# Kernel optimization log

Hardware: AMD Instinct MI355X
Metric: run time of the kernel (lower is better)

Reference implementation:

```python
import jax, jax.numpy as jnp
import numpy as np

N = 100000      # nodes
E = 640000      # directed edges (before self-loops)
F_IN = 128      # num_features
C1 = 64         # latent_size (conv1 out, heads=1)
C2 = 16         # num_classes (conv2 out, heads=1)
NEG_SLOPE = 0.2


def setup_inputs() -> dict:
    key = jax.random.key(0)
    ks = jax.random.split(key, 10)
    s = 0.1
    return {
        "x": jax.random.normal(ks[0], (N, F_IN), jnp.float32),
        "edge_index": jax.random.randint(ks[1], (2, E), 0, N, dtype=jnp.int32),
        "W1": jax.random.normal(ks[2], (F_IN, C1), jnp.float32) * s,
        "att_src1": jax.random.normal(ks[3], (C1,), jnp.float32) * s,
        "att_dst1": jax.random.normal(ks[4], (C1,), jnp.float32) * s,
        "b1": jax.random.normal(ks[5], (C1,), jnp.float32) * s,
        "W2": jax.random.normal(ks[6], (C1, C2), jnp.float32) * s,
        "att_src2": jax.random.normal(ks[7], (C2,), jnp.float32) * s,
        "att_dst2": jax.random.normal(ks[8], (C2,), jnp.float32) * s,
        "b2": jax.random.normal(ks[9], (C2,), jnp.float32) * s,
    }


def gat_layer(x, src, dst, W, a_src, a_dst, b, n_nodes):
    # x: [N, F] -> h: [N, C] (heads=1)
    h = x @ W
    # per-edge attention logits: alpha_j + alpha_i, then leaky_relu
    alpha = jax.nn.leaky_relu((h @ a_src)[src] + (h @ a_dst)[dst], NEG_SLOPE)
    # scatter-softmax over destination-node groups (numerically stable)
    amax = jax.ops.segment_max(alpha, dst, num_segments=n_nodes)
    e = jnp.exp(alpha - amax[dst])
    denom = jax.ops.segment_sum(e, dst, num_segments=n_nodes)
    w = e / (denom[dst] + 1e-16)
    # gather src features, weight, scatter-add to dst
    out = jax.ops.segment_sum(h[src] * w[:, None], dst, num_segments=n_nodes)
    return out + b


def kl_to_std_normal(out):
    # GIB reparameterize: mean = out[:, :ceil(C/2)], std = softplus(out[:, -ceil(C/2):])
    size = (out.shape[-1] + 1) // 2
    mean = out[:, :size]
    std = jax.nn.softplus(out[:, -size:]) + 1e-10
    kl = -jnp.log(std) + 0.5 * (std * std + mean * mean - 1.0)
    return kl.reshape(out.shape[0], -1, 1)  # [N, size, heads=1]


def reference(x, edge_index, W1, att_src1, att_dst1, b1, W2, att_src2, att_dst2, b2):
    n = x.shape[0]
    loop = jnp.arange(n, dtype=edge_index.dtype)  # PyG GATConv add_self_loops=True
    src = jnp.concatenate([edge_index[0], loop])
    dst = jnp.concatenate([edge_index[1], loop])

    out1 = gat_layer(x, src, dst, W1, att_src1, att_dst1, b1, n)
    ixz1 = kl_to_std_normal(out1)

    h = jax.nn.elu(out1)  # dropout is a no-op in eval mode
    out2 = gat_layer(h, src, dst, W2, att_src2, att_dst2, b2, n)
    ixz2 = kl_to_std_normal(out2)

    return (out2, ixz1, ixz2)
```

## Files before the change

kernel.cpp:

```cpp
#include <hip/hip_runtime.h>
#include <math.h>

#define NN 100000
#define NE 640000
#define FIN 128
#define C1 64
#define C2 16
#define NEG_SLOPE 0.2f
#define SLOTS 32
#define G1_BLOCKS ((NN + 127) / 128)
#define SORT_EPB 2048
#define SORT_NBLK ((NE + SORT_EPB - 1) / SORT_EPB)
#define NBUCK 512
#define NBUCK_USED ((NN + 255) / 256)

typedef unsigned int uint32;
typedef __attribute__((ext_vector_type(8))) short bf16x8;
typedef __attribute__((ext_vector_type(4))) float f32x4;

static __device__ __forceinline__ float lrelu(float x) { return x > 0.f ? x : NEG_SLOPE * x; }
static __device__ __forceinline__ float softplusn(float x) {
    return fmaxf(x, 0.f) + __logf(1.f + __expf(-fabsf(x)));
}
static __device__ __forceinline__ unsigned short f2bf(float f) {
    uint32 u = __float_as_uint(f);
    u += 0x7fffu + ((u >> 16) & 1u);
    return (unsigned short)(u >> 16);
}
static __device__ __forceinline__ float bf2f_lo(uint32 p) { return __uint_as_float(p << 16); }
static __device__ __forceinline__ float bf2f_hi(uint32 p) { return __uint_as_float(p & 0xffff0000u); }

#define G1T 2
__global__ __launch_bounds__(256, 3) void k_gemm1(
        const float* __restrict__ x, const float* __restrict__ W1,
        const float* __restrict__ attS, const float* __restrict__ attD,
        unsigned short* __restrict__ h1b, float* __restrict__ as1, float* __restrict__ ad1) {
    __shared__ uint32 ts[4][16][36];
    int lane = threadIdx.x & 63;
    int wv = threadIdx.x >> 6;
    int col = lane & 15;
    int g = lane >> 4;
    int wbase = (blockIdx.x * 4 + wv) * (G1T * 16);
    if (wbase >= NN) return;

    bf16x8 bfr[4][4];
#pragma unroll
    for (int t = 0; t < 4; t++)
#pragma unroll
        for (int j = 0; j < 4; j++) {
            int c = col + j * 16;
#pragma unroll
            for (int i = 0; i < 8; i++)
                bfr[t][j][i] = (short)f2bf(W1[(t * 32 + g * 8 + i) * C1 + c]);
        }
    float ats[4], atd[4];
#pragma unroll
    for (int j = 0; j < 4; j++) { ats[j] = attS[col + j * 16]; atd[j] = attD[col + j * 16]; }

    for (int tl = 0; tl < G1T; tl++) {
        int tbase = wbase + tl * 16;
        int arow = tbase + col; if (arow > NN - 1) arow = NN - 1;
        const float* xr = &x[(size_t)arow * FIN];
        float4 f0[4], f1[4];
#pragma unroll
        for (int t = 0; t < 4; t++) {
            f0[t] = *reinterpret_cast<const float4*>(&xr[t * 32 + g * 8]);
            f1[t] = *reinterpret_cast<const float4*>(&xr[t * 32 + g * 8 + 4]);
        }
        bf16x8 a[4];
#pragma unroll
        for (int t = 0; t < 4; t++) {
            a[t][0] = (short)f2bf(f0[t].x); a[t][1] = (short)f2bf(f0[t].y);
            a[t][2] = (short)f2bf(f0[t].z); a[t][3] = (short)f2bf(f0[t].w);
            a[t][4] = (short)f2bf(f1[t].x); a[t][5] = (short)f2bf(f1[t].y);
            a[t][6] = (short)f2bf(f1[t].z); a[t][7] = (short)f2bf(f1[t].w);
        }
        f32x4 acc[4];
#pragma unroll
        for (int j = 0; j < 4; j++) acc[j] = (f32x4){0.f, 0.f, 0.f, 0.f};
#pragma unroll
        for (int t = 0; t < 4; t++)
#pragma unroll
            for (int j = 0; j < 4; j++)
                acc[j] = __builtin_amdgcn_mfma_f32_16x16x32_bf16(a[t], bfr[t][j], acc[j], 0, 0, 0);

        float sA[4] = {0.f, 0.f, 0.f, 0.f}, sD[4] = {0.f, 0.f, 0.f, 0.f};
        unsigned short* tsw = (unsigned short*)&ts[wv][0][0];
#pragma unroll
        for (int reg = 0; reg < 4; reg++) {
            int trow = g * 4 + reg;
#pragma unroll
            for (int j = 0; j < 4; j++) {
                float v = acc[j][reg];
                tsw[trow * 72 + col + j * 16] = f2bf(v);
                sA[reg] = fmaf(v, ats[j], sA[reg]);
                sD[reg] = fmaf(v, atd[j], sD[reg]);
            }
        }
        __builtin_amdgcn_wave_barrier();
        {
            int rrow = lane >> 2, rq = lane & 3;
            uint4 w0 = *reinterpret_cast<const uint4*>(&ts[wv][rrow][rq * 8]);
            uint4 w1 = *reinterpret_cast<const uint4*>(&ts[wv][rrow][rq * 8 + 4]);
            int orow = tbase + rrow;
            if (orow < NN) {
                unsigned short* op = &h1b[(size_t)orow * C1 + rq * 16];
                *reinterpret_cast<uint4*>(op) = w0;
                *reinterpret_cast<uint4*>(op + 8) = w1;
            }
        }
        __builtin_amdgcn_wave_barrier();
#pragma unroll
        for (int off = 8; off; off >>= 1)
#pragma unroll
            for (int reg = 0; reg < 4; reg++) {
                sA[reg] += __shfl_xor(sA[reg], off);
                sD[reg] += __shfl_xor(sD[reg], off);
            }
        if (col == 0) {
#pragma unroll
            for (int reg = 0; reg < 4; reg++) {
                int row = tbase + g * 4 + reg;
                if (row < NN) { as1[row] = sA[reg]; ad1[row] = sD[reg]; }
            }
        }
    }
}

__global__ __launch_bounds__(256) void k_hist(const int* __restrict__ ei, int* __restrict__ blockHist) {
    __shared__ int lh[NBUCK];
    int t = threadIdx.x;
    for (int i = t; i < NBUCK; i += 256) lh[i] = 0;
    __syncthreads();
    int base = blockIdx.x * SORT_EPB;
#pragma unroll
    for (int k = 0; k < 8; k++) {
        int e = base + k * 256 + t;
        if (e < NE) atomicAdd(&lh[ei[NE + e] >> 8], 1);
    }
    __syncthreads();
    for (int i = t; i < NBUCK; i += 256) blockHist[i * SORT_NBLK + blockIdx.x] = lh[i];
}

__global__ __launch_bounds__(256) void k_scan(int* __restrict__ blockHist, int* __restrict__ bucketCnt) {
    __shared__ int s[SORT_NBLK];
    int b = blockIdx.x, t = threadIdx.x;
    for (int i = t; i < SORT_NBLK; i += 256) s[i] = blockHist[b * SORT_NBLK + i];
    __syncthreads();
    for (int d = 1; d < SORT_NBLK; d <<= 1) {
        int i0 = t, i1 = t + 256;
        int v0 = 0, v1 = 0;
        if (i0 >= d && i0 < SORT_NBLK) v0 = s[i0 - d];
        if (i1 >= d && i1 < SORT_NBLK) v1 = s[i1 - d];
        __syncthreads();
        if (i0 >= d && i0 < SORT_NBLK) s[i0] += v0;
        if (i1 >= d && i1 < SORT_NBLK) s[i1] += v1;
        __syncthreads();
    }
    for (int i = t; i < SORT_NBLK; i += 256)
        blockHist[b * SORT_NBLK + i] = (i == 0) ? 0 : s[i - 1];
    if (t == 0) bucketCnt[b] = s[SORT_NBLK - 1];
}

__global__ __launch_bounds__(256) void k_scat1(const int* __restrict__ ei,
        const int* __restrict__ blockHist, uint2* __restrict__ ebuf) {
    __shared__ int lh[NBUCK];
    int t = threadIdx.x;
    for (int i = t; i < NBUCK; i += 256) lh[i] = 0;
    __syncthreads();
    int base = blockIdx.x * SORT_EPB;
#pragma unroll
    for (int k = 0; k < 8; k++) {
        int e = base + k * 256 + t;
        if (e < NE) {
            int src = ei[e], dst = ei[NE + e];
            int bin = dst >> 8;
            int rank = atomicAdd(&lh[bin], 1);
            int pos = bin * SORT_EPB + blockHist[bin * SORT_NBLK + blockIdx.x] + rank;
            ebuf[pos] = make_uint2((uint32)src, (uint32)dst);
        }
    }
}

__global__ __launch_bounds__(256) void k_csr(const uint2* __restrict__ ebuf,
        const int* __restrict__ bucketCnt, int* __restrict__ cnt, int* __restrict__ csr32) {
    __shared__ int lcnt[256];
    __shared__ int lcsr[256 * SLOTS];
    int t = threadIdx.x, b = blockIdx.x;
    if (t < 256) lcnt[t] = 0;
    for (int i = t; i < 256 * SLOTS; i += 256) lcsr[i] = 0;
    __syncthreads();
    int n = bucketCnt[b];
    if (n > SORT_EPB) n = SORT_EPB;
    for (int i = t; i < n; i += 256) {
        uint2 e = ebuf[b * SORT_EPB + i];
        int ln = (int)(e.y & 255u);
        int pos = atomicAdd(&lcnt[ln], 1);
        if (pos < SLOTS) lcsr[ln * SLOTS + pos] = (int)e.x;
    }
    __syncthreads();
    int node0 = b * 256;
    for (int i = t; i < 256 * SLOTS; i += 256) {
        int node = node0 + (i >> 5);
        if (node < NN) csr32[(size_t)node0 * SLOTS + i] = lcsr[i];
    }
    if (node0 + t < NN) cnt[node0 + t] = lcnt[t];
}

__global__ __launch_bounds__(256, 4) void k_agg1(
        const int* __restrict__ cnt, const int* __restrict__ csr32,
        const float* __restrict__ as1, const float* __restrict__ ad1,
        const unsigned short* __restrict__ h1b, const float* __restrict__ b1,
        unsigned short* __restrict__ heb, float* __restrict__ ixz1) {
    int lane = threadIdx.x & 63;
    int wid = (blockIdx.x * blockDim.x + threadIdx.x) >> 6;
    int grp = lane >> 4, gl = lane & 15;
    int gbase = grp << 4;
    int node = wid * 4 + grp;
    if (node >= NN) return;
    int base = node * SLOTS;
    int dcnt = cnt[node];
    int s_l = csr32[base + gl];
    int4 S0 = *reinterpret_cast<const int4*>(&csr32[base]);
    int4 S1 = *reinterpret_cast<const int4*>(&csr32[base + 4]);
    int4 S2 = *reinterpret_cast<const int4*>(&csr32[base + 8]);
    int4 S3 = *reinterpret_cast<const int4*>(&csr32[base + 12]);
    float adn = ad1[node];
    float asn = as1[node];
    float asv = as1[s_l];
    float4 o;

    if (dcnt <= 16) {
        float al = (gl < dcnt) ? lrelu(asv + adn) : -1e30f;
        float wl = __expf(al);
        float den = wl;
#pragma unroll
        for (int off = 8; off; off >>= 1) den += __shfl_xor(den, off);
        float wself = __expf(lrelu(asn + adn));
        den += wself;
        float inv = __builtin_amdgcn_rcpf(den + 1e-16f);
        wl *= inv; wself *= inv;
        const unsigned short* hb = h1b + gl * 4;
        uint2 PS  = *reinterpret_cast<const uint2*>(&hb[(size_t)node * C1]);
        uint2 P0  = *reinterpret_cast<const uint2*>(&hb[(size_t)S0.x * C1]);
        uint2 P1  = *reinterpret_cast<const uint2*>(&hb[(size_t)S0.y * C1]);
        uint2 P2  = *reinterpret_cast<const uint2*>(&hb[(size_t)S0.z * C1]);
        uint2 P3  = *reinterpret_cast<const uint2*>(&hb[(size_t)S0.w * C1]);
        uint2 P4  = *reinterpret_cast<const uint2*>(&hb[(size_t)S1.x * C1]);
        uint2 P5  = *reinterpret_cast<const uint2*>(&hb[(size_t)S1.y * C1]);
        uint2 P6  = *reinterpret_cast<const uint2*>(&hb[(size_t)S1.z * C1]);
        uint2 P7  = *reinterpret_cast<const uint2*>(&hb[(size_t)S1.w * C1]);
        uint2 P8  = *reinterpret_cast<const uint2*>(&hb[(size_t)S2.x * C1]);
        uint2 P9  = *reinterpret_cast<const uint2*>(&hb[(size_t)S2.y * C1]);
        uint2 P10 = *reinterpret_cast<const uint2*>(&hb[(size_t)S2.z * C1]);
        uint2 P11 = *reinterpret_cast<const uint2*>(&hb[(size_t)S2.w * C1]);
        uint2 P12 = *reinterpret_cast<const uint2*>(&hb[(size_t)S3.x * C1]);
        uint2 P13 = *reinterpret_cast<const uint2*>(&hb[(size_t)S3.y * C1]);
        uint2 P14 = *reinterpret_cast<const uint2*>(&hb[(size_t)S3.z * C1]);
        uint2 P15 = *reinterpret_cast<const uint2*>(&hb[(size_t)S3.w * C1]);
        float4 acc;
        acc.x = wself * bf2f_lo(PS.x);
        acc.y = wself * bf2f_hi(PS.x);
        acc.z = wself * bf2f_lo(PS.y);
        acc.w = wself * bf2f_hi(PS.y);
#define ACC1(k, Pk) { float w = __shfl(wl, gbase | k); \
        acc.x = fmaf(w, bf2f_lo(Pk.x), acc.x); acc.y = fmaf(w, bf2f_hi(Pk.x), acc.y); \
        acc.z = fmaf(w, bf2f_lo(Pk.y), acc.z); acc.w = fmaf(w, bf2f_hi(Pk.y), acc.w); }
        ACC1(0, P0)  ACC1(1, P1)  ACC1(2, P2)  ACC1(3, P3)
        ACC1(4, P4)  ACC1(5, P5)  ACC1(6, P6)  ACC1(7, P7)
        ACC1(8, P8)  ACC1(9, P9)  ACC1(10, P10) ACC1(11, P11)
        ACC1(12, P12) ACC1(13, P13) ACC1(14, P14) ACC1(15, P15)
#undef ACC1
        o = acc;
    } else {
        int dcl = dcnt < SLOTS ? dcnt : SLOTS;
        float aself = lrelu(asn + adn);
        float m = aself;
        for (int e = gl; e < dcl; e += 16) m = fmaxf(m, lrelu(as1[csr32[base + e]] + adn));
#pragma unroll
        for (int off = 8; off; off >>= 1) m = fmaxf(m, __shfl_xor(m, off));
        float den = 0.f;
        for (int e = gl; e < dcl; e += 16) den += __expf(lrelu(as1[csr32[base + e]] + adn) - m);
#pragma unroll
        for (int off = 8; off; off >>= 1) den += __shfl_xor(den, off);
        den += __expf(aself - m);
        float inv = __builtin_amdgcn_rcpf(den + 1e-16f);
        float wsf = __expf(aself - m) * inv;
        uint2 ps = *reinterpret_cast<const uint2*>(&h1b[(size_t)node * C1 + gl * 4]);
        float4 acc;
        acc.x = wsf * bf2f_lo(ps.x);
        acc.y = wsf * bf2f_hi(ps.x);
        acc.z = wsf * bf2f_lo(ps.y);
        acc.w = wsf * bf2f_hi(ps.y);
        for (int e = 0; e < dcl; e++) {
            int s = csr32[base + e];
            float wgt = __expf(lrelu(as1[s] + adn) - m) * inv;
            uint2 p = *reinterpret_cast<const uint2*>(&h1b[(size_t)s * C1 + gl * 4]);
            acc.x = fmaf(wgt, bf2f_lo(p.x), acc.x);
            acc.y = fmaf(wgt, bf2f_hi(p.x), acc.y);
            acc.z = fmaf(wgt, bf2f_lo(p.y), acc.z);
            acc.w = fmaf(wgt, bf2f_hi(p.y), acc.w);
        }
        o = acc;
    }
    float4 bv = *reinterpret_cast<const float4*>(&b1[gl * 4]);
    o.x += bv.x; o.y += bv.y; o.z += bv.z; o.w += bv.w;
    float4 he;
    he.x = o.x > 0.f ? o.x : __expf(o.x) - 1.f;
    he.y = o.y > 0.f ? o.y : __expf(o.y) - 1.f;
    he.z = o.z > 0.f ? o.z : __expf(o.z) - 1.f;
    he.w = o.w > 0.f ? o.w : __expf(o.w) - 1.f;
    uint2 hw;
    hw.x = (uint32)f2bf(he.x) | ((uint32)f2bf(he.y) << 16);
    hw.y = (uint32)f2bf(he.z) | ((uint32)f2bf(he.w) << 16);
    *reinterpret_cast<uint2*>(&heb[(size_t)node * C1 + gl * 4]) = hw;
    float4 oth;
    oth.x = __shfl_down(o.x, 8);
    oth.y = __shfl_down(o.y, 8);
    oth.z = __shfl_down(o.z, 8);
    oth.w = __shfl_down(o.w, 8);
    if (gl < 8) {
        float4 kl; float sd;
        sd = softplusn(oth.x) + 1e-10f; kl.x = -__logf(sd) + 0.5f * (sd * sd + o.x * o.x - 1.f);
        sd = softplusn(oth.y) + 1e-10f; kl.y = -__logf(sd) + 0.5f * (sd * sd + o.y * o.y - 1.f);
        sd = softplusn(oth.z) + 1e-10f; kl.z = -__logf(sd) + 0.5f * (sd * sd + o.z * o.z - 1.f);
        sd = softplusn(oth.w) + 1e-10f; kl.w = -__logf(sd) + 0.5f * (sd * sd + o.w * o.w - 1.f);
        *reinterpret_cast<float4*>(&ixz1[(size_t)node * 32 + gl * 4]) = kl;
    }
}

#define G2T 4
__global__ __launch_bounds__(256, 4) void k_gemm2(
        const unsigned short* __restrict__ heb, const float* __restrict__ W2,
        const float* __restrict__ attS, const float* __restrict__ attD,
        unsigned short* __restrict__ h2b, float* __restrict__ as2, float* __restrict__ ad2) {
    int lane = threadIdx.x & 63;
    int wv = threadIdx.x >> 6;
    int col = lane & 15, g = lane >> 4;
    int wbase = (blockIdx.x * 4 + wv) * (G2T * 16);
    if (wbase >= NN) return;
    bf16x8 bfr[2];
#pragma unroll
    for (int t = 0; t < 2; t++)
#pragma unroll
        for (int i = 0; i < 8; i++)
            bfr[t][i] = (short)f2bf(W2[(t * 32 + g * 8 + i) * C2 + col]);
    float ats = attS[col], atd = attD[col];
#pragma unroll
    for (int tl = 0; tl < G2T; tl++) {
        int tbase = wbase + tl * 16;
        if (tbase >= NN) break;
        int arow = tbase + col; if (arow > NN - 1) arow = NN - 1;
        bf16x8 a0 = *reinterpret_cast<const bf16x8*>(&heb[(size_t)arow * C1 + g * 8]);
        bf16x8 a1 = *reinterpret_cast<const bf16x8*>(&heb[(size_t)arow * C1 + 32 + g * 8]);
        f32x4 acc = (f32x4){0.f, 0.f, 0.f, 0.f};
        acc = __builtin_amdgcn_mfma_f32_16x16x32_bf16(a0, bfr[0], acc, 0, 0, 0);
        acc = __builtin_amdgcn_mfma_f32_16x16x32_bf16(a1, bfr[1], acc, 0, 0, 0);
        float sA[4], sD[4];
#pragma unroll
        for (int reg = 0; reg < 4; reg++) {
            int row = tbase + g * 4 + reg;
            if (row < NN) h2b[(size_t)row * C2 + col] = f2bf(acc[reg]);
            sA[reg] = acc[reg] * ats;
            sD[reg] = acc[reg] * atd;
        }
#pragma unroll
        for (int off = 8; off; off >>= 1)
#pragma unroll
            for (int reg = 0; reg < 4; reg++) {
                sA[reg] += __shfl_xor(sA[reg], off);
                sD[reg] += __shfl_xor(sD[reg], off);
            }
        if (col == 0) {
#pragma unroll
            for (int reg = 0; reg < 4; reg++) {
                int row = tbase + g * 4 + reg;
                if (row < NN) { as2[row] = sA[reg]; ad2[row] = sD[reg]; }
            }
        }
    }
}

__global__ __launch_bounds__(256, 8) void k_agg2(
        const int* __restrict__ cnt, const int* __restrict__ csr32,
        const float* __restrict__ as2, const float* __restrict__ ad2,
        const unsigned short* __restrict__ h2b, const float* __restrict__ b2,
        float* __restrict__ out2, float* __restrict__ ixz2) {
    int lane = threadIdx.x & 63;
    int wid = (blockIdx.x * blockDim.x + threadIdx.x) >> 6;
    int grp = lane >> 4, gl = lane & 15;
    int gbase = grp << 4;
    int node = wid * 4 + grp;
    if (node >= NN) return;
    int base = node * SLOTS;
    int f4 = gl & 3, eg = gl >> 2;
    int dcnt = cnt[node];
    int s_l = csr32[base + gl];
    int sk0 = csr32[base + eg];
    int sk1 = csr32[base + 4 + eg];
    int sk2 = csr32[base + 8 + eg];
    int sk3 = csr32[base + 12 + eg];
    float adn = ad2[node];
    float asn = as2[node];
    float asv = as2[s_l];
    float out;

    if (dcnt <= 16) {
        float al = (gl < dcnt) ? lrelu(asv + adn) : -1e30f;
        float wl = __expf(al);
        float den = wl;
#pragma unroll
        for (int off = 8; off; off >>= 1) den += __shfl_xor(den, off);
        float wself = __expf(lrelu(asn + adn));
        den += wself;
        float inv = __builtin_amdgcn_rcpf(den + 1e-16f);
        wl *= inv; wself *= inv;
        uint2 PS = *reinterpret_cast<const uint2*>(&h2b[(size_t)node * C2 + f4 * 4]);
        uint2 P0 = *reinterpret_cast<const uint2*>(&h2b[(size_t)sk0 * C2 + f4 * 4]);
        uint2 P1 = *reinterpret_cast<const uint2*>(&h2b[(size_t)sk1 * C2 + f4 * 4]);
        uint2 P2 = *reinterpret_cast<const uint2*>(&h2b[(size_t)sk2 * C2 + f4 * 4]);
        uint2 P3 = *reinterpret_cast<const uint2*>(&h2b[(size_t)sk3 * C2 + f4 * 4]);
        float ws = (eg == 0) ? wself : 0.f;
        float4 acc;
        acc.x = ws * bf2f_lo(PS.x);
        acc.y = ws * bf2f_hi(PS.x);
        acc.z = ws * bf2f_lo(PS.y);
        acc.w = ws * bf2f_hi(PS.y);
        float w0 = __shfl(wl, gbase | eg);
        float w1 = __shfl(wl, gbase | (4 + eg));
        float w2 = __shfl(wl, gbase | (8 + eg));
        float w3 = __shfl(wl, gbase | (12 + eg));
        acc.x = fmaf(w0, bf2f_lo(P0.x), acc.x);
        acc.y = fmaf(w0, bf2f_hi(P0.x), acc.y);
        acc.z = fmaf(w0, bf2f_lo(P0.y), acc.z);
        acc.w = fmaf(w0, bf2f_hi(P0.y), acc.w);
        acc.x = fmaf(w1, bf2f_lo(P1.x), acc.x);
        acc.y = fmaf(w1, bf2f_hi(P1.x), acc.y);
        acc.z = fmaf(w1, bf2f_lo(P1.y), acc.z);
        acc.w = fmaf(w1, bf2f_hi(P1.y), acc.w);
        acc.x = fmaf(w2, bf2f_lo(P2.x), acc.x);
        acc.y = fmaf(w2, bf2f_hi(P2.x), acc.y);
        acc.z = fmaf(w2, bf2f_lo(P2.y), acc.z);
        acc.w = fmaf(w2, bf2f_hi(P2.y), acc.w);
        acc.x = fmaf(w3, bf2f_lo(P3.x), acc.x);
        acc.y = fmaf(w3, bf2f_hi(P3.x), acc.y);
        acc.z = fmaf(w3, bf2f_lo(P3.y), acc.z);
        acc.w = fmaf(w3, bf2f_hi(P3.y), acc.w);
#pragma unroll
        for (int off = 4; off <= 8; off <<= 1) {
            acc.x += __shfl_xor(acc.x, off);
            acc.y += __shfl_xor(acc.y, off);
            acc.z += __shfl_xor(acc.z, off);
            acc.w += __shfl_xor(acc.w, off);
        }
        int srcl = gbase | (gl >> 2);
        float t0 = __shfl(acc.x, srcl);
        float t1 = __shfl(acc.y, srcl);
        float t2 = __shfl(acc.z, srcl);
        float t3 = __shfl(acc.w, srcl);
        float t01 = (gl & 1) ? t1 : t0;
        float t23 = (gl & 1) ? t3 : t2;
        out = (gl & 2) ? t23 : t01;
    } else {
        int dcl = dcnt < SLOTS ? dcnt : SLOTS;
        float aself = lrelu(asn + adn);
        float m = aself;
        for (int e = gl; e < dcl; e += 16) m = fmaxf(m, lrelu(as2[csr32[base + e]] + adn));
#pragma unroll
        for (int off = 8; off; off >>= 1) m = fmaxf(m, __shfl_xor(m, off));
        float den = 0.f;
        for (int e = gl; e < dcl; e += 16) den += __expf(lrelu(as2[csr32[base + e]] + adn) - m);
#pragma unroll
        for (int off = 8; off; off >>= 1) den += __shfl_xor(den, off);
        den += __expf(aself - m);
        float inv = __builtin_amdgcn_rcpf(den + 1e-16f);
        float wsf = __expf(aself - m) * inv;
        float acc = wsf * __uint_as_float(((uint32)h2b[(size_t)node * C2 + gl]) << 16);
        for (int e = 0; e < dcl; e++) {
            int s = csr32[base + e];
            float wgt = __expf(lrelu(as2[s] + adn) - m) * inv;
            acc = fmaf(wgt, __uint_as_float(((uint32)h2b[(size_t)s * C2 + gl]) << 16), acc);
        }
        out = acc;
    }
    out += b2[gl];
    out2[(size_t)node * C2 + gl] = out;
    float other = __shfl_down(out, 8);
    if (gl < 8) {
        float sd = softplusn(other) + 1e-10f;
        float kl = -__logf(sd) + 0.5f * (sd * sd + out * out - 1.f);
        ixz2[(size_t)node * 8 + gl] = kl;
    }
}

extern "C" void kernel_launch(void* const* d_in, const int* in_sizes, int n_in,
                              void* d_out, int out_size, void* d_ws, size_t ws_size,
                              hipStream_t stream) {
    const float* x     = (const float*)d_in[0];
    const int*   ei    = (const int*)d_in[1];
    const float* W1    = (const float*)d_in[2];
    const float* aS1   = (const float*)d_in[3];
    const float* aD1   = (const float*)d_in[4];
    const float* b1    = (const float*)d_in[5];
    const float* W2    = (const float*)d_in[6];
    const float* aS2   = (const float*)d_in[7];
    const float* aD2   = (const float*)d_in[8];
    const float* b2    = (const float*)d_in[9];

    float* out = (float*)d_out;
    float* out2 = out;
    float* ixz1 = out + (size_t)NN * C2;
    float* ixz2 = ixz1 + (size_t)NN * 32;

    char* p = (char*)d_ws;
    auto alloc = [&](size_t bytes) -> void* {
        void* r = (void*)p;
        p += (bytes + 255) & ~(size_t)255;
        return r;
    };
    int* cnt        = (int*)alloc((size_t)NN * 4);
    int* csr32      = (int*)alloc((size_t)NN * SLOTS * 4);
    int* blockHist  = (int*)alloc((size_t)NBUCK * SORT_NBLK * 4);
    int* bucketCnt  = (int*)alloc((size_t)NBUCK * 4);
    uint2* ebuf     = (uint2*)alloc((size_t)NBUCK * SORT_EPB * 8);
    unsigned short* h1b = (unsigned short*)alloc((size_t)NN * C1 * 2);
    float* as1   = (float*)alloc((size_t)NN * 4);
    float* ad1   = (float*)alloc((size_t)NN * 4);
    unsigned short* heb = (unsigned short*)alloc((size_t)NN * C1 * 2);
    unsigned short* h2b = (unsigned short*)alloc((size_t)NN * C2 * 2);
    float* as2   = (float*)alloc((size_t)NN * 4);
    float* ad2   = (float*)alloc((size_t)NN * 4);
    (void)ws_size; (void)in_sizes; (void)n_in; (void)out_size;

    k_gemm1<<<G1_BLOCKS, 256, 0, stream>>>(x, W1, aS1, aD1, h1b, as1, ad1);

    k_hist <<<SORT_NBLK, 256, 0, stream>>>(ei, blockHist);
    k_scan <<<NBUCK, 256, 0, stream>>>(blockHist, bucketCnt);
    k_scat1<<<SORT_NBLK, 256, 0, stream>>>(ei, blockHist, ebuf);
    k_csr  <<<NBUCK_USED, 256, 0, stream>>>(ebuf, bucketCnt, cnt, csr32);

    k_agg1<<<(NN + 15) / 16, 256, 0, stream>>>(cnt, csr32, as1, ad1, h1b, b1, heb, ixz1);

    k_gemm2<<<(NN + 4 * G2T * 16 - 1) / (4 * G2T * 16), 256, 0, stream>>>(heb, W2, aS2, aD2, h2b, as2, ad2);
    k_agg2<<<(NN + 15) / 16, 256, 0, stream>>>(cnt, csr32, as2, ad2, h2b, b2, out2, ixz2);
}
```

Measured before the change: 106.2 us.

## Fuse edge histogram into GEMM1 launch and pack edge buffer entries to 32 bits

The histogram kernel now runs as extra blocks appended to the first GEMM launch, which removes one kernel launch and lets the two independent workloads overlap. The scatter kernel seeds its shared-memory counters with the per-block offsets, so it no longer re-reads the global offset table for every edge. Each edge is packed into one 32-bit word (source shifted left by 8, low 8 bits of the destination), which halves the intermediate buffer's traffic. The shared-memory histogram array raises the GEMM blocks' LDS footprint, which could lower their occupancy, and the packing relies on source ids fitting in 24 bits.

```diff
diff --git a/kernel.cpp b/kernel.cpp
--- a/kernel.cpp
+++ b/kernel.cpp
@@ -31,11 +31,28 @@
 static __device__ __forceinline__ float bf2f_hi(uint32 p) { return __uint_as_float(p & 0xffff0000u); }
 
 #define G1T 2
-__global__ __launch_bounds__(256, 3) void k_gemm1(
+__global__ __launch_bounds__(256, 3) void k_g1hist(
         const float* __restrict__ x, const float* __restrict__ W1,
         const float* __restrict__ attS, const float* __restrict__ attD,
-        unsigned short* __restrict__ h1b, float* __restrict__ as1, float* __restrict__ ad1) {
+        unsigned short* __restrict__ h1b, float* __restrict__ as1, float* __restrict__ ad1,
+        const int* __restrict__ ei, int* __restrict__ blockHist) {
     __shared__ uint32 ts[4][16][36];
+    __shared__ int lh[NBUCK];
+    if (blockIdx.x >= G1_BLOCKS) {
+        int blk = (int)blockIdx.x - G1_BLOCKS;
+        int t = threadIdx.x;
+        for (int i = t; i < NBUCK; i += 256) lh[i] = 0;
+        __syncthreads();
+        int base = blk * SORT_EPB;
+#pragma unroll
+        for (int k = 0; k < 8; k++) {
+            int e = base + k * 256 + t;
+            if (e < NE) atomicAdd(&lh[ei[NE + e] >> 8], 1);
+        }
+        __syncthreads();
+        for (int i = t; i < NBUCK; i += 256) blockHist[i * SORT_NBLK + blk] = lh[i];
+        return;
+    }
     int lane = threadIdx.x & 63;
     int wv = threadIdx.x >> 6;
     int col = lane & 15;
@@ -125,21 +142,6 @@
             }
         }
     }
-}
-
-__global__ __launch_bounds__(256) void k_hist(const int* __restrict__ ei, int* __restrict__ blockHist) {
-    __shared__ int lh[NBUCK];
-    int t = threadIdx.x;
-    for (int i = t; i < NBUCK; i += 256) lh[i] = 0;
-    __syncthreads();
-    int base = blockIdx.x * SORT_EPB;
-#pragma unroll
-    for (int k = 0; k < 8; k++) {
-        int e = base + k * 256 + t;
-        if (e < NE) atomicAdd(&lh[ei[NE + e] >> 8], 1);
-    }
-    __syncthreads();
-    for (int i = t; i < NBUCK; i += 256) blockHist[i * SORT_NBLK + blockIdx.x] = lh[i];
 }
 
 __global__ __launch_bounds__(256) void k_scan(int* __restrict__ blockHist, int* __restrict__ bucketCnt) {
@@ -163,10 +165,10 @@
 }
 
 __global__ __launch_bounds__(256) void k_scat1(const int* __restrict__ ei,
-        const int* __restrict__ blockHist, uint2* __restrict__ ebuf) {
+        const int* __restrict__ blockHist, uint32* __restrict__ ebuf) {
     __shared__ int lh[NBUCK];
     int t = threadIdx.x;
-    for (int i = t; i < NBUCK; i += 256) lh[i] = 0;
+    for (int i = t; i < NBUCK; i += 256) lh[i] = blockHist[i * SORT_NBLK + blockIdx.x];
     __syncthreads();
     int base = blockIdx.x * SORT_EPB;
 #pragma unroll
@@ -175,28 +177,27 @@
         if (e < NE) {
             int src = ei[e], dst = ei[NE + e];
             int bin = dst >> 8;
-            int rank = atomicAdd(&lh[bin], 1);
-            int pos = bin * SORT_EPB + blockHist[bin * SORT_NBLK + blockIdx.x] + rank;
-            ebuf[pos] = make_uint2((uint32)src, (uint32)dst);
-        }
-    }
-}
-
-__global__ __launch_bounds__(256) void k_csr(const uint2* __restrict__ ebuf,
+            int pos = atomicAdd(&lh[bin], 1);
+            ebuf[bin * SORT_EPB + pos] = ((uint32)src << 8) | (uint32)(dst & 255);
+        }
+    }
+}
+
+__global__ __launch_bounds__(256) void k_csr(const uint32* __restrict__ ebuf,
         const int* __restrict__ bucketCnt, int* __restrict__ cnt, int* __restrict__ csr32) {
     __shared__ int lcnt[256];
     __shared__ int lcsr[256 * SLOTS];
     int t = threadIdx.x, b = blockIdx.x;
-    if (t < 256) lcnt[t] = 0;
+    lcnt[t] = 0;
     for (int i = t; i < 256 * SLOTS; i += 256) lcsr[i] = 0;
     __syncthreads();
     int n = bucketCnt[b];
     if (n > SORT_EPB) n = SORT_EPB;
     for (int i = t; i < n; i += 256) {
-        uint2 e = ebuf[b * SORT_EPB + i];
-        int ln = (int)(e.y & 255u);
+        uint32 e = ebuf[b * SORT_EPB + i];
+        int ln = (int)(e & 255u);
         int pos = atomicAdd(&lcnt[ln], 1);
-        if (pos < SLOTS) lcsr[ln * SLOTS + pos] = (int)e.x;
+        if (pos < SLOTS) lcsr[ln * SLOTS + pos] = (int)(e >> 8);
     }
     __syncthreads();
     int node0 = b * 256;
@@ -522,7 +523,7 @@
     int* csr32      = (int*)alloc((size_t)NN * SLOTS * 4);
     int* blockHist  = (int*)alloc((size_t)NBUCK * SORT_NBLK * 4);
     int* bucketCnt  = (int*)alloc((size_t)NBUCK * 4);
-    uint2* ebuf     = (uint2*)alloc((size_t)NBUCK * SORT_EPB * 8);
+    uint32* ebuf    = (uint32*)alloc((size_t)NBUCK * SORT_EPB * 4);
     unsigned short* h1b = (unsigned short*)alloc((size_t)NN * C1 * 2);
     float* as1   = (float*)alloc((size_t)NN * 4);
     float* ad1   = (float*)alloc((size_t)NN * 4);
@@ -532,9 +533,8 @@
     float* ad2   = (float*)alloc((size_t)NN * 4);
     (void)ws_size; (void)in_sizes; (void)n_in; (void)out_size;
 
-    k_gemm1<<<G1_BLOCKS, 256, 0, stream>>>(x, W1, aS1, aD1, h1b, as1, ad1);
-
-    k_hist <<<SORT_NBLK, 256, 0, stream>>>(ei, blockHist);
+    k_g1hist<<<G1_BLOCKS + SORT_NBLK, 256, 0, stream>>>(x, W1, aS1, aD1, h1b, as1, ad1, ei, blockHist);
+
     k_scan <<<NBUCK, 256, 0, stream>>>(blockHist, bucketCnt);
     k_scat1<<<SORT_NBLK, 256, 0, stream>>>(ei, blockHist, ebuf);
     k_csr  <<<NBUCK_USED, 256, 0, stream>>>(ebuf, bucketCnt, cnt, csr32);
```

After: 99.74 us. -6.1%, faster.
